# Kernel optimization log

Hardware: AMD Instinct MI355X
Metric: run time of the kernel (lower is better)

The kernel has to match this reference:

```python
import jax, jax.numpy as jnp
import numpy as np

BIG = 1e30  # finite 'inf' so masked-min keeps clean gradients

def setup_inputs() -> dict:
    key = jax.random.key(0)
    k1, k2, k3, k4 = jax.random.split(key, 4)
    B, N, C = 8, 2048, 3
    pred = jax.random.normal(k1, (B, N, C), dtype=jnp.float32)
    target = jax.random.normal(k2, (B, N, C), dtype=jnp.float32)
    points = jax.random.normal(k3, (B, N, C), dtype=jnp.float32)
    mask = jax.random.randint(k4, (B, N), 0, 2, dtype=jnp.int32)
    return {"pred": pred, "target": target, "mask": mask, "points": points}

def _loss(pred, target, points, maskf):
    # masked L1 term: per-point mean over xyz, masked mean over valid points
    l1_map = jnp.mean(jnp.abs(pred - target), axis=2) * maskf      # [B,N]
    l1 = l1_map.sum() / maskf.sum()

    clean = points + target                                        # [B,N,3]
    predp = points + pred                                          # [B,N,3]
    # pairwise L1 distances between clean (rows) and pred (cols)
    D = jnp.sum(jnp.abs(clean[:, :, None, :] - predp[:, None, :, :]), axis=-1)  # [B,N,N]

    valid_cnt = maskf.sum(axis=1)                                  # [B]
    # clean -> nearest valid pred point (mask columns j)
    min_x = jnp.min(jnp.where(maskf[:, None, :] > 0, D, BIG), axis=2)  # [B,N]
    # pred -> nearest valid clean point (mask rows i)
    min_y = jnp.min(jnp.where(maskf[:, :, None] > 0, D, BIG), axis=1)  # [B,N]
    cham = (min_x * maskf).sum(axis=1) / valid_cnt \
         + (min_y * maskf).sum(axis=1) / valid_cnt                 # [B]
    cd = cham.mean()  # per-batch chamfer summed then divided by B

    # converging_to == 'chamfer'
    return l1 + jnp.exp(-l1) * cd

def reference(pred, target, mask, points):
    maskf = mask.astype(pred.dtype)
    return _loss(pred, target, points, maskf)
```

## Files before the change

### kernel.cpp

```cpp
#include <hip/hip_runtime.h>
#include <math.h>
#include <float.h>

#define BB 8
#define NN 2048
#define BN (BB * NN)
#define BLK 256
#define Q 2
#define QSPLIT 4
#define QSLICE (BLK * Q)
#define CSPLIT 16
#define CCHUNK (NN / CSPLIT)

#define MINPART_FLOATS (CSPLIT * 2 * BN)

__global__ __launch_bounds__(BLK) void k_main(const float* __restrict__ pred,
                                              const float* __restrict__ target,
                                              const float* __restrict__ points,
                                              const int* __restrict__ mask,
                                              float* __restrict__ minpart,
                                              float* __restrict__ l1part,
                                              float* __restrict__ cntpart,
                                              unsigned int* __restrict__ counter) {
    int bid = blockIdx.x;
    int cs = bid & (CSPLIT - 1);
    int qs = (bid >> 4) & (QSPLIT - 1);
    int b = (bid >> 6) & 7;
    int task = bid >> 9;
    int t = threadIdx.x;

    if (bid == 0 && t == 0) *counter = 0u;

    const float* dq = task ? pred : target;
    const float* dc = task ? target : pred;

    __shared__ float4 cand[CCHUNK];
    if (t < CCHUNK) {
        int g = b * NN + cs * CCHUNK + t;
        size_t g3 = (size_t)g * 3;
        float x = 1e30f, y = 1e30f, z = 1e30f;
        if (mask[g]) {
            x = points[g3 + 0] + dc[g3 + 0];
            y = points[g3 + 1] + dc[g3 + 1];
            z = points[g3 + 2] + dc[g3 + 2];
        }
        cand[t] = make_float4(x, y, z, 0.f);
    }
    __syncthreads();

    float qx[Q], qy[Q], qz[Q], mn[Q];
    #pragma unroll
    for (int q = 0; q < Q; ++q) {
        int qi = qs * QSLICE + q * BLK + t;
        size_t g3 = (size_t)(b * NN + qi) * 3;
        qx[q] = points[g3 + 0] + dq[g3 + 0];
        qy[q] = points[g3 + 1] + dq[g3 + 1];
        qz[q] = points[g3 + 2] + dq[g3 + 2];
        mn[q] = FLT_MAX;
    }

    #pragma unroll 8
    for (int j = 0; j < CCHUNK; j += 2) {
        float4 c0 = cand[j];
        float4 c1 = cand[j + 1];
        #pragma unroll
        for (int q = 0; q < Q; ++q) {
            float d0 = fabsf(qx[q] - c0.x) + fabsf(qy[q] - c0.y) + fabsf(qz[q] - c0.z);
            float d1 = fabsf(qx[q] - c1.x) + fabsf(qy[q] - c1.y) + fabsf(qz[q] - c1.z);
            mn[q] = fminf(fminf(d0, d1), mn[q]);
        }
    }

    float* mp = minpart + (size_t)cs * (2 * BN) + (size_t)task * BN + b * NN;
    #pragma unroll
    for (int q = 0; q < Q; ++q)
        mp[qs * QSLICE + q * BLK + t] = mn[q];

    if (task == 0 && cs == 0) {
        float s = 0.f, c = 0.f;
        #pragma unroll
        for (int q = 0; q < Q; ++q) {
            int gi = b * NN + qs * QSLICE + q * BLK + t;
            size_t g3 = (size_t)gi * 3;
            float m = (float)mask[gi];
            s += (fabsf(pred[g3 + 0] - target[g3 + 0]) +
                  fabsf(pred[g3 + 1] - target[g3 + 1]) +
                  fabsf(pred[g3 + 2] - target[g3 + 2])) * (1.0f / 3.0f) * m;
            c += m;
        }
        for (int off = 32; off; off >>= 1) {
            s += __shfl_down(s, off, 64);
            c += __shfl_down(c, off, 64);
        }
        __shared__ float ls[4], lc[4];
        if ((t & 63) == 0) { ls[t >> 6] = s; lc[t >> 6] = c; }
        __syncthreads();
        if (t == 0) {
            l1part[b * QSPLIT + qs]  = ls[0] + ls[1] + ls[2] + ls[3];
            cntpart[b * QSPLIT + qs] = lc[0] + lc[1] + lc[2] + lc[3];
        }
    }
}

__global__ __launch_bounds__(BLK) void k_redfin(const float* __restrict__ minpart,
                                                const int* __restrict__ mask,
                                                const float* __restrict__ l1part,
                                                const float* __restrict__ cntpart,
                                                float* __restrict__ champart,
                                                unsigned int* __restrict__ counter,
                                                float* __restrict__ out) {
    int tb = blockIdx.x;
    int s8 = tb & 7;
    int b = (tb >> 3) & 7;
    int task = tb >> 6;
    int t = threadIdx.x;

    int qi = s8 * BLK + t;
    size_t idx = (size_t)task * BN + b * NN + qi;
    float mn = minpart[idx];
    #pragma unroll
    for (int cs = 1; cs < CSPLIT; ++cs)
        mn = fminf(mn, minpart[(size_t)cs * (2 * BN) + idx]);
    float v = mn * (float)mask[b * NN + qi];

    for (int off = 32; off; off >>= 1) v += __shfl_down(v, off, 64);

    __shared__ float ls[4];
    __shared__ int isLast;
    __shared__ float ch[128];
    if ((t & 63) == 0) ls[t >> 6] = v;
    __syncthreads();
    if (t == 0) {
        float bs = ls[0] + ls[1] + ls[2] + ls[3];
        __hip_atomic_store(&champart[tb], bs, __ATOMIC_RELEASE, __HIP_MEMORY_SCOPE_AGENT);
        int ticket = __hip_atomic_fetch_add(counter, 1u, __ATOMIC_ACQ_REL, __HIP_MEMORY_SCOPE_AGENT);
        isLast = (ticket == 127);
    }
    __syncthreads();
    if (!isLast) return;

    if (t < 128) ch[t] = __hip_atomic_load(&champart[t], __ATOMIC_ACQUIRE, __HIP_MEMORY_SCOPE_AGENT);
    __syncthreads();
    if (t == 0) {
        double cnt[BB], msum = 0.0, l1num = 0.0;
        for (int b2 = 0; b2 < BB; ++b2) {
            double cb = 0.0;
            for (int k = 0; k < QSPLIT; ++k) {
                cb += (double)cntpart[b2 * QSPLIT + k];
                l1num += (double)l1part[b2 * QSPLIT + k];
            }
            cnt[b2] = cb;
            msum += cb;
        }
        double l1 = l1num / msum;
        double cd = 0.0;
        for (int b2 = 0; b2 < BB; ++b2) {
            double chb = 0.0;
            for (int tk = 0; tk < 2; ++tk)
                for (int s = 0; s < 8; ++s)
                    chb += (double)ch[tk * 64 + b2 * 8 + s];
            cd += chb / cnt[b2];
        }
        cd *= (1.0 / BB);
        out[0] = (float)(l1 + exp(-l1) * cd);
    }
}

extern "C" void kernel_launch(void* const* d_in, const int* in_sizes, int n_in,
                              void* d_out, int out_size, void* d_ws, size_t ws_size,
                              hipStream_t stream) {
    const float* pred   = (const float*)d_in[0];
    const float* target = (const float*)d_in[1];
    const int*   mask   = (const int*)d_in[2];
    const float* points = (const float*)d_in[3];
    float* out = (float*)d_out;

    float* minpart  = (float*)d_ws;
    char* tail = (char*)d_ws + (size_t)MINPART_FLOATS * 4;
    float* champart = (float*)tail;
    float* l1part   = (float*)(tail + 512);
    float* cntpart  = (float*)(tail + 640);
    unsigned int* counter = (unsigned int*)(tail + 768);

    k_main<<<2 * BB * QSPLIT * CSPLIT, BLK, 0, stream>>>(pred, target, points, mask,
                                                         minpart, l1part, cntpart, counter);
    k_redfin<<<128, BLK, 0, stream>>>(minpart, mask, l1part, cntpart,
                                      champart, counter, out);
}
```

Before: 23.64 us.

## Compact valid query and candidate points per block to skip masked work

Each block now uses ballot and popcount to pack only the masked-valid query points and candidate points into shared memory, then computes distances only over those compacted lists. With roughly half the points masked, this cuts the pairwise distance work to about a quarter. Each block now owns one query per thread instead of two, so the grid doubles. The compaction adds an extra synchronisation and leaves divergent tail threads. Minpart entries for invalid queries are left unwritten, so the reducer now selects on the mask instead of multiplying, which avoids NaN or garbage from stale values.

```diff
diff --git a/kernel.cpp b/kernel.cpp
--- a/kernel.cpp
+++ b/kernel.cpp
@@ -6,11 +6,10 @@
 #define NN 2048
 #define BN (BB * NN)
 #define BLK 256
-#define Q 2
-#define QSPLIT 4
-#define QSLICE (BLK * Q)
+#define QSPLIT 8
+#define QSLICE 256
 #define CSPLIT 16
-#define CCHUNK (NN / CSPLIT)
+#define CCHUNK 128
 
 #define MINPART_FLOATS (CSPLIT * 2 * BN)
 
@@ -25,80 +24,98 @@
     int bid = blockIdx.x;
     int cs = bid & (CSPLIT - 1);
     int qs = (bid >> 4) & (QSPLIT - 1);
-    int b = (bid >> 6) & 7;
-    int task = bid >> 9;
+    int b = (bid >> 7) & 7;
+    int task = bid >> 10;
     int t = threadIdx.x;
+    int lane = t & 63, w = t >> 6;
 
     if (bid == 0 && t == 0) *counter = 0u;
 
     const float* dq = task ? pred : target;
     const float* dc = task ? target : pred;
 
-    __shared__ float4 cand[CCHUNK];
-    if (t < CCHUNK) {
-        int g = b * NN + cs * CCHUNK + t;
-        size_t g3 = (size_t)g * 3;
-        float x = 1e30f, y = 1e30f, z = 1e30f;
-        if (mask[g]) {
-            x = points[g3 + 0] + dc[g3 + 0];
-            y = points[g3 + 1] + dc[g3 + 1];
-            z = points[g3 + 2] + dc[g3 + 2];
-        }
-        cand[t] = make_float4(x, y, z, 0.f);
-    }
-    __syncthreads();
-
-    float qx[Q], qy[Q], qz[Q], mn[Q];
-    #pragma unroll
-    for (int q = 0; q < Q; ++q) {
-        int qi = qs * QSLICE + q * BLK + t;
-        size_t g3 = (size_t)(b * NN + qi) * 3;
-        qx[q] = points[g3 + 0] + dq[g3 + 0];
-        qy[q] = points[g3 + 1] + dq[g3 + 1];
-        qz[q] = points[g3 + 2] + dq[g3 + 2];
-        mn[q] = FLT_MAX;
-    }
-
-    #pragma unroll 8
-    for (int j = 0; j < CCHUNK; j += 2) {
-        float4 c0 = cand[j];
-        float4 c1 = cand[j + 1];
-        #pragma unroll
-        for (int q = 0; q < Q; ++q) {
-            float d0 = fabsf(qx[q] - c0.x) + fabsf(qy[q] - c0.y) + fabsf(qz[q] - c0.z);
-            float d1 = fabsf(qx[q] - c1.x) + fabsf(qy[q] - c1.y) + fabsf(qz[q] - c1.z);
-            mn[q] = fminf(fminf(d0, d1), mn[q]);
-        }
-    }
-
-    float* mp = minpart + (size_t)cs * (2 * BN) + (size_t)task * BN + b * NN;
-    #pragma unroll
-    for (int q = 0; q < Q; ++q)
-        mp[qs * QSLICE + q * BLK + t] = mn[q];
+    __shared__ float4 cand[CCHUNK + 8];
+    __shared__ float qlx[BLK], qly[BLK], qlz[BLK];
+    __shared__ unsigned char qidx[BLK];
+    __shared__ int cnts[8];
+
+    int gq = b * NN + qs * QSLICE + t;
+    size_t gq3 = (size_t)gq * 3;
+    int qm = mask[gq];
+    float qx = points[gq3 + 0] + dq[gq3 + 0];
+    float qy = points[gq3 + 1] + dq[gq3 + 1];
+    float qz = points[gq3 + 2] + dq[gq3 + 2];
 
     if (task == 0 && cs == 0) {
-        float s = 0.f, c = 0.f;
-        #pragma unroll
-        for (int q = 0; q < Q; ++q) {
-            int gi = b * NN + qs * QSLICE + q * BLK + t;
-            size_t g3 = (size_t)gi * 3;
-            float m = (float)mask[gi];
-            s += (fabsf(pred[g3 + 0] - target[g3 + 0]) +
-                  fabsf(pred[g3 + 1] - target[g3 + 1]) +
-                  fabsf(pred[g3 + 2] - target[g3 + 2])) * (1.0f / 3.0f) * m;
-            c += m;
-        }
+        float m = (float)qm;
+        float s = (fabsf(pred[gq3 + 0] - target[gq3 + 0]) +
+                   fabsf(pred[gq3 + 1] - target[gq3 + 1]) +
+                   fabsf(pred[gq3 + 2] - target[gq3 + 2])) * (1.0f / 3.0f) * m;
+        float c = m;
         for (int off = 32; off; off >>= 1) {
             s += __shfl_down(s, off, 64);
             c += __shfl_down(c, off, 64);
         }
         __shared__ float ls[4], lc[4];
-        if ((t & 63) == 0) { ls[t >> 6] = s; lc[t >> 6] = c; }
+        if (lane == 0) { ls[w] = s; lc[w] = c; }
         __syncthreads();
         if (t == 0) {
             l1part[b * QSPLIT + qs]  = ls[0] + ls[1] + ls[2] + ls[3];
             cntpart[b * QSPLIT + qs] = lc[0] + lc[1] + lc[2] + lc[3];
         }
+    }
+
+    unsigned long long balq = __ballot(qm != 0);
+    int myq = __popcll(balq & ((1ull << lane) - 1));
+    if (lane == 0) cnts[w] = __popcll(balq);
+
+    int cm = 0;
+    float cx = 0.f, cy = 0.f, cz = 0.f;
+    if (t < CCHUNK) {
+        int g = b * NN + cs * CCHUNK + t;
+        size_t g3 = (size_t)g * 3;
+        cm = mask[g];
+        if (cm) {
+            cx = points[g3 + 0] + dc[g3 + 0];
+            cy = points[g3 + 1] + dc[g3 + 1];
+            cz = points[g3 + 2] + dc[g3 + 2];
+        }
+    }
+    unsigned long long balc = __ballot(cm != 0);
+    int myc = __popcll(balc & ((1ull << lane) - 1));
+    if (t < CCHUNK && lane == 0) cnts[4 + w] = __popcll(balc);
+    __syncthreads();
+
+    int nQ = cnts[0] + cnts[1] + cnts[2] + cnts[3];
+    int nC = cnts[4] + cnts[5];
+    int qbase = 0;
+    for (int i = 0; i < w; ++i) qbase += cnts[i];
+    if (qm) {
+        int s = qbase + myq;
+        qlx[s] = qx; qly[s] = qy; qlz[s] = qz;
+        qidx[s] = (unsigned char)t;
+    }
+    if (t < CCHUNK && cm) {
+        int s = (w ? cnts[4] : 0) + myc;
+        cand[s] = make_float4(cx, cy, cz, 0.f);
+    }
+    int nCp = (nC + 7) & ~7;
+    if (t < nCp - nC) cand[nC + t] = make_float4(1e30f, 1e30f, 1e30f, 0.f);
+    __syncthreads();
+
+    if (t < nQ) {
+        float ax = qlx[t], ay = qly[t], az = qlz[t];
+        float mn = FLT_MAX;
+        #pragma unroll 4
+        for (int j = 0; j < nCp; j += 2) {
+            float4 c0 = cand[j];
+            float4 c1 = cand[j + 1];
+            float d0 = fabsf(ax - c0.x) + fabsf(ay - c0.y) + fabsf(az - c0.z);
+            float d1 = fabsf(ax - c1.x) + fabsf(ay - c1.y) + fabsf(az - c1.z);
+            mn = fminf(fminf(d0, d1), mn);
+        }
+        minpart[(size_t)cs * (2 * BN) + (size_t)task * BN + b * NN
+                + qs * QSLICE + qidx[t]] = mn;
     }
 }
 
@@ -121,7 +138,7 @@
     #pragma unroll
     for (int cs = 1; cs < CSPLIT; ++cs)
         mn = fminf(mn, minpart[(size_t)cs * (2 * BN) + idx]);
-    float v = mn * (float)mask[b * NN + qi];
+    float v = (mask[b * NN + qi] != 0) ? mn : 0.f;
 
     for (int off = 32; off; off >>= 1) v += __shfl_down(v, off, 64);
 
@@ -179,8 +196,8 @@
     char* tail = (char*)d_ws + (size_t)MINPART_FLOATS * 4;
     float* champart = (float*)tail;
     float* l1part   = (float*)(tail + 512);
-    float* cntpart  = (float*)(tail + 640);
-    unsigned int* counter = (unsigned int*)(tail + 768);
+    float* cntpart  = (float*)(tail + 768);
+    unsigned int* counter = (unsigned int*)(tail + 1024);
 
     k_main<<<2 * BB * QSPLIT * CSPLIT, BLK, 0, stream>>>(pred, target, points, mask,
                                                          minpart, l1part, cntpart, counter);
```

After: 26.42 us. 11.8% more time.

## Rebalance query/candidate split and vectorize loads, stores and reduction

Applied to the files above, without the earlier changes.

Each thread now handles four query points and the candidate set is split 64 ways instead of 16, so the main kernel launches 2048 blocks, each with a 32-candidate chunk. Query coordinates, masked-L1 inputs and per-chunk minima are read and written as float4 or int4. The reduction kernel drops to 32 blocks, each thread combining 64 partial minima with float4 loads. The counter reset is gone; the last block is detected with a modulo ticket, which assumes the counter starts at a multiple of 32. The price is four times more partial-minimum traffic to the workspace and a longer serial min-reduction on fewer blocks.

```diff
diff --git a/kernel.cpp b/kernel.cpp
--- a/kernel.cpp
+++ b/kernel.cpp
@@ -6,11 +6,13 @@
 #define NN 2048
 #define BN (BB * NN)
 #define BLK 256
-#define Q 2
-#define QSPLIT 4
+#define Q 4
+#define QSPLIT 2
 #define QSLICE (BLK * Q)
-#define CSPLIT 16
+#define CSPLIT 64
 #define CCHUNK (NN / CSPLIT)
+#define NBLOCKS (2 * BB * QSPLIT * CSPLIT)
+#define RBLOCKS 32
 
 #define MINPART_FLOATS (CSPLIT * 2 * BN)
 
@@ -20,16 +22,13 @@
                                               const int* __restrict__ mask,
                                               float* __restrict__ minpart,
                                               float* __restrict__ l1part,
-                                              float* __restrict__ cntpart,
-                                              unsigned int* __restrict__ counter) {
+                                              float* __restrict__ cntpart) {
     int bid = blockIdx.x;
     int cs = bid & (CSPLIT - 1);
-    int qs = (bid >> 4) & (QSPLIT - 1);
-    int b = (bid >> 6) & 7;
-    int task = bid >> 9;
+    int qs = (bid >> 6) & (QSPLIT - 1);
+    int b = (bid >> 7) & 7;
+    int task = bid >> 10;
     int t = threadIdx.x;
-
-    if (bid == 0 && t == 0) *counter = 0u;
 
     const float* dq = task ? pred : target;
     const float* dc = task ? target : pred;
@@ -48,15 +47,20 @@
     }
     __syncthreads();
 
+    int qi0 = qs * QSLICE + 4 * t;
     float qx[Q], qy[Q], qz[Q], mn[Q];
-    #pragma unroll
-    for (int q = 0; q < Q; ++q) {
-        int qi = qs * QSLICE + q * BLK + t;
-        size_t g3 = (size_t)(b * NN + qi) * 3;
-        qx[q] = points[g3 + 0] + dq[g3 + 0];
-        qy[q] = points[g3 + 1] + dq[g3 + 1];
-        qz[q] = points[g3 + 2] + dq[g3 + 2];
-        mn[q] = FLT_MAX;
+    {
+        size_t g3 = (size_t)(b * NN + qi0) * 3;
+        const float4* p4 = (const float4*)(points + g3);
+        const float4* d4 = (const float4*)(dq + g3);
+        float4 a0 = p4[0], a1 = p4[1], a2 = p4[2];
+        float4 e0 = d4[0], e1 = d4[1], e2 = d4[2];
+        qx[0] = a0.x + e0.x; qy[0] = a0.y + e0.y; qz[0] = a0.z + e0.z;
+        qx[1] = a0.w + e0.w; qy[1] = a1.x + e1.x; qz[1] = a1.y + e1.y;
+        qx[2] = a1.z + e1.z; qy[2] = a1.w + e1.w; qz[2] = a2.x + e2.x;
+        qx[3] = a2.y + e2.y; qy[3] = a2.z + e2.z; qz[3] = a2.w + e2.w;
+        #pragma unroll
+        for (int q = 0; q < Q; ++q) mn[q] = FLT_MAX;
     }
 
     #pragma unroll 8
@@ -71,23 +75,27 @@
         }
     }
 
-    float* mp = minpart + (size_t)cs * (2 * BN) + (size_t)task * BN + b * NN;
-    #pragma unroll
-    for (int q = 0; q < Q; ++q)
-        mp[qs * QSLICE + q * BLK + t] = mn[q];
+    {
+        float* mp = minpart + (size_t)cs * (2 * BN) + (size_t)task * BN + b * NN + qi0;
+        *(float4*)mp = make_float4(mn[0], mn[1], mn[2], mn[3]);
+    }
 
     if (task == 0 && cs == 0) {
+        size_t g3 = (size_t)(b * NN + qi0) * 3;
+        const float4* p4 = (const float4*)(pred + g3);
+        const float4* t4 = (const float4*)(target + g3);
+        const int4 m4 = *(const int4*)(mask + b * NN + qi0);
+        float4 u0 = p4[0], u1 = p4[1], u2 = p4[2];
+        float4 v0 = t4[0], v1 = t4[1], v2 = t4[2];
+        float mf[Q] = { (float)m4.x, (float)m4.y, (float)m4.z, (float)m4.w };
+        float l[Q];
+        l[0] = fabsf(u0.x - v0.x) + fabsf(u0.y - v0.y) + fabsf(u0.z - v0.z);
+        l[1] = fabsf(u0.w - v0.w) + fabsf(u1.x - v1.x) + fabsf(u1.y - v1.y);
+        l[2] = fabsf(u1.z - v1.z) + fabsf(u1.w - v1.w) + fabsf(u2.x - v2.x);
+        l[3] = fabsf(u2.y - v2.y) + fabsf(u2.z - v2.z) + fabsf(u2.w - v2.w);
         float s = 0.f, c = 0.f;
         #pragma unroll
-        for (int q = 0; q < Q; ++q) {
-            int gi = b * NN + qs * QSLICE + q * BLK + t;
-            size_t g3 = (size_t)gi * 3;
-            float m = (float)mask[gi];
-            s += (fabsf(pred[g3 + 0] - target[g3 + 0]) +
-                  fabsf(pred[g3 + 1] - target[g3 + 1]) +
-                  fabsf(pred[g3 + 2] - target[g3 + 2])) * (1.0f / 3.0f) * m;
-            c += m;
-        }
+        for (int q = 0; q < Q; ++q) { s += l[q] * (1.0f / 3.0f) * mf[q]; c += mf[q]; }
         for (int off = 32; off; off >>= 1) {
             s += __shfl_down(s, off, 64);
             c += __shfl_down(c, off, 64);
@@ -107,39 +115,42 @@
                                                 const float* __restrict__ l1part,
                                                 const float* __restrict__ cntpart,
                                                 float* __restrict__ champart,
-                                                unsigned int* __restrict__ counter,
+                                                unsigned int* __restrict__ gcnt,
                                                 float* __restrict__ out) {
-    int tb = blockIdx.x;
-    int s8 = tb & 7;
-    int b = (tb >> 3) & 7;
-    int task = tb >> 6;
+    int bid = blockIdx.x;
     int t = threadIdx.x;
+    int q0 = bid * 1024 + 4 * t;
 
-    int qi = s8 * BLK + t;
-    size_t idx = (size_t)task * BN + b * NN + qi;
-    float mn = minpart[idx];
+    float4 m0 = *(const float4*)(minpart + q0);
     #pragma unroll
-    for (int cs = 1; cs < CSPLIT; ++cs)
-        mn = fminf(mn, minpart[(size_t)cs * (2 * BN) + idx]);
-    float v = mn * (float)mask[b * NN + qi];
+    for (int p = 1; p < CSPLIT; ++p) {
+        float4 mp = *(const float4*)(minpart + (size_t)p * (2 * BN) + q0);
+        m0.x = fminf(m0.x, mp.x); m0.y = fminf(m0.y, mp.y);
+        m0.z = fminf(m0.z, mp.z); m0.w = fminf(m0.w, mp.w);
+    }
+    const int4 m4 = *(const int4*)(mask + (q0 & (BN - 1)));
+    float v = (m4.x ? m0.x : 0.f) + (m4.y ? m0.y : 0.f)
+            + (m4.z ? m0.z : 0.f) + (m4.w ? m0.w : 0.f);
 
     for (int off = 32; off; off >>= 1) v += __shfl_down(v, off, 64);
 
-    __shared__ float ls[4];
+    __shared__ float fls[4];
     __shared__ int isLast;
-    __shared__ float ch[128];
-    if ((t & 63) == 0) ls[t >> 6] = v;
+    __shared__ float ch[RBLOCKS];
+    if ((t & 63) == 0) fls[t >> 6] = v;
     __syncthreads();
     if (t == 0) {
-        float bs = ls[0] + ls[1] + ls[2] + ls[3];
-        __hip_atomic_store(&champart[tb], bs, __ATOMIC_RELEASE, __HIP_MEMORY_SCOPE_AGENT);
-        int ticket = __hip_atomic_fetch_add(counter, 1u, __ATOMIC_ACQ_REL, __HIP_MEMORY_SCOPE_AGENT);
-        isLast = (ticket == 127);
+        float bs = fls[0] + fls[1] + fls[2] + fls[3];
+        __hip_atomic_store(&champart[bid], bs, __ATOMIC_RELEASE, __HIP_MEMORY_SCOPE_AGENT);
+        unsigned int tk = __hip_atomic_fetch_add(gcnt, 1u, __ATOMIC_ACQ_REL,
+                                                 __HIP_MEMORY_SCOPE_AGENT);
+        isLast = (((tk + 1u) & (RBLOCKS - 1)) == 0u);
     }
     __syncthreads();
     if (!isLast) return;
 
-    if (t < 128) ch[t] = __hip_atomic_load(&champart[t], __ATOMIC_ACQUIRE, __HIP_MEMORY_SCOPE_AGENT);
+    if (t < RBLOCKS)
+        ch[t] = __hip_atomic_load(&champart[t], __ATOMIC_ACQUIRE, __HIP_MEMORY_SCOPE_AGENT);
     __syncthreads();
     if (t == 0) {
         double cnt[BB], msum = 0.0, l1num = 0.0;
@@ -155,10 +166,8 @@
         double l1 = l1num / msum;
         double cd = 0.0;
         for (int b2 = 0; b2 < BB; ++b2) {
-            double chb = 0.0;
-            for (int tk = 0; tk < 2; ++tk)
-                for (int s = 0; s < 8; ++s)
-                    chb += (double)ch[tk * 64 + b2 * 8 + s];
+            double chb = (double)ch[(b2 << 1)] + (double)ch[(b2 << 1) | 1]
+                       + (double)ch[16 | (b2 << 1)] + (double)ch[16 | (b2 << 1) | 1];
             cd += chb / cnt[b2];
         }
         cd *= (1.0 / BB);
@@ -178,12 +187,12 @@
     float* minpart  = (float*)d_ws;
     char* tail = (char*)d_ws + (size_t)MINPART_FLOATS * 4;
     float* champart = (float*)tail;
-    float* l1part   = (float*)(tail + 512);
-    float* cntpart  = (float*)(tail + 640);
-    unsigned int* counter = (unsigned int*)(tail + 768);
+    float* l1part   = (float*)(tail + 128);
+    float* cntpart  = (float*)(tail + 192);
+    unsigned int* gcnt = (unsigned int*)(tail + 256);
 
-    k_main<<<2 * BB * QSPLIT * CSPLIT, BLK, 0, stream>>>(pred, target, points, mask,
-                                                         minpart, l1part, cntpart, counter);
-    k_redfin<<<128, BLK, 0, stream>>>(minpart, mask, l1part, cntpart,
-                                      champart, counter, out);
+    k_main<<<NBLOCKS, BLK, 0, stream>>>(pred, target, points, mask,
+                                        minpart, l1part, cntpart);
+    k_redfin<<<RBLOCKS, BLK, 0, stream>>>(minpart, mask, l1part, cntpart,
+                                          champart, gcnt, out);
 }
```

After: 23.35 us. About the same (-1.2%).
